# Kernel optimization log

Measured on AMD Instinct MI355X. Metric: run time of the kernel, lower is better.

## Reference

```python
import jax, jax.numpy as jnp
import numpy as np
from jax import lax

# SLAYER neuron / simulation constants (from netParams)
THETA = 10.0       # spike threshold
TAU_SR = 10.0      # synaptic (PSP) time constant
TAU_REF = 1.0      # refractory time constant
SCALE_REF = 2.0    # refractory scale
TAU_RHO = 1.0      # surrogate-gradient width (unused in fwd)
K_PSP = 32         # truncation length of SRM alpha kernel
K_REF = 16         # truncation length of refractory kernel

_t = np.arange(K_PSP, dtype=np.float64)
PSP_KERN = jnp.asarray((_t / TAU_SR) * np.exp(1.0 - _t / TAU_SR), jnp.float32)  # [K_PSP]
_tr = np.arange(1, K_REF + 1, dtype=np.float64)
REF_KERN = jnp.asarray(-SCALE_REF * THETA * (_tr / TAU_REF) * np.exp(1.0 - _tr / TAU_REF), jnp.float32)  # [K_REF]


def psp(x):
    """Causal temporal FIR filter with SRM alpha kernel; x: [..., T]."""
    sh = x.shape
    T = sh[-1]
    flat = x.reshape(-1, 1, T)                       # [B*, 1, T]
    k = PSP_KERN[::-1][None, None, :]                # correlation kernel (reversed)
    y = lax.conv_general_dilated(flat, k, (1,), [(K_PSP - 1, 0)])
    return y.reshape(sh)


def spike(u):
    """Threshold with refractory feedback, sequential over time. u: [..., T]."""
    uT = jnp.moveaxis(u, -1, 0)                      # [T, ...]
    buf0 = jnp.zeros(u.shape[:-1] + (K_REF,), u.dtype)

    def step(buf, ut):
        v = ut + buf[..., 0]
        s = (v >= THETA).astype(u.dtype)
        buf = jnp.concatenate([buf[..., 1:], jnp.zeros_like(buf[..., :1])], -1)
        buf = buf + s[..., None] * REF_KERN
        return buf, s

    _, sT = lax.scan(step, buf0, uT)
    return jnp.moveaxis(sT, 0, -1)


def conv_t(x, w, stride, pad):
    """2D conv applied independently per timestep. x: [N,C,H,W,T], w: [Co,C,kh,kw]."""
    N, C, H, W, T = x.shape
    xt = jnp.moveaxis(x, -1, 1).reshape(N * T, C, H, W)
    y = lax.conv_general_dilated(xt, w, (stride, stride), [(pad, pad), (pad, pad)])
    Co, Ho, Wo = y.shape[1], y.shape[2], y.shape[3]
    return jnp.moveaxis(y.reshape(N, T, Co, Ho, Wo), 1, -1)


def pool_t(x):
    """SLAYER sum-pool 2x2/s2 with weight 1.1*theta/kernel_area. x: [N,C,H,W,T]."""
    s = lax.reduce_window(x, np.float32(0.0), lax.add, (1, 1, 2, 2, 1), (1, 1, 2, 2, 1), 'VALID')
    return s * np.float32(1.1 * THETA / 4.0)


def setup_inputs() -> dict:
    key = jax.random.key(0)
    ks = jax.random.split(key, 5)
    spikeInput = (jax.random.uniform(ks[0], (4, 2, 256, 256, 50)) < 0.02).astype(jnp.float32)
    w1 = jax.random.normal(ks[1], (8, 2, 5, 5), jnp.float32) * 2.0
    w2 = jax.random.normal(ks[2], (16, 8, 3, 3), jnp.float32) * 1.5
    w3 = jax.random.normal(ks[3], (32, 16, 3, 3), jnp.float32) * 1.5
    w_fc = jax.random.normal(ks[4], (2, 32, 8, 8), jnp.float32) * 0.3
    return {"spikeInput": spikeInput, "w1": w1, "w2": w2, "w3": w3, "w_fc": w_fc}


def reference(spikeInput, w1, w2, w3, w_fc):
    x = spike(conv_t(psp(spikeInput), w1, 2, 1))   # [4,8,127,127,50]
    x = spike(pool_t(psp(x)))                      # [4,8,63,63,50]
    x = spike(conv_t(psp(x), w2, 2, 1))            # [4,16,32,32,50]
    x = spike(pool_t(psp(x)))                      # [4,16,16,16,50]
    x = spike(conv_t(psp(x), w3, 2, 1))            # [4,32,8,8,50]
    u = psp(x)
    out = jnp.einsum('ochw,nchwt->not', w_fc, u)   # dense over (C,H,W)
    return spike(out[:, :, None, None, :])         # [4,2,1,1,50]
```

## Files before the change

### kernel.cpp

```cpp
#include <hip/hip_runtime.h>
#include <cmath>

struct K32 { float k[32]; };
struct K16 { float k[16]; };

#define THETA 10.0f

__global__ __launch_bounds__(128)
void psp_kernel(const float* __restrict__ in, float* __restrict__ out,
                int nrows, K32 pk) {
  __shared__ __align__(16) float lds[64 * 50];
  const int rowBase = blockIdx.x * 64;
  const int tid = threadIdx.x;
  const int vr = min(64, nrows - rowBase);
  const int n4 = (vr * 50) >> 2;
  const float4* g4 = (const float4*)(in + (size_t)rowBase * 50);
  for (int i = tid; i < n4; i += 128) *(float4*)(&lds[4 * i]) = g4[i];
  __syncthreads();
  const int r = tid & 63;
  const int part = tid >> 6;
  const bool act = r < vr;
  float x[50];
  if (act) {
    if (part == 0) {
#pragma unroll
      for (int t = 0; t < 25; ++t) x[t] = lds[r * 50 + t];
    } else {
#pragma unroll
      for (int t = 0; t < 50; ++t) x[t] = lds[r * 50 + t];
    }
  }
  __syncthreads();
  if (act) {
    if (part == 0) {
#pragma unroll
      for (int t = 0; t < 25; ++t) {
        float a = 0.f;
#pragma unroll
        for (int k = 31; k >= 0; --k)
          if (t - k >= 0) a += x[t - k] * pk.k[k];
        lds[r * 50 + t] = a;
      }
    } else {
#pragma unroll
      for (int t = 25; t < 50; ++t) {
        float a = 0.f;
#pragma unroll
        for (int k = 31; k >= 0; --k)
          if (t - k >= 0) a += x[t - k] * pk.k[k];
        lds[r * 50 + t] = a;
      }
    }
  }
  __syncthreads();
  float4* o4 = (float4*)(out + (size_t)rowBase * 50);
  for (int i = tid; i < n4; i += 128) o4[i] = *(const float4*)(&lds[4 * i]);
}

template <int CIN, int COUT, int KK, int HIN, int WIN, int S1H, int S1W,
          int S2H, int S2W>
__global__ __launch_bounds__(256)
void conv_pps_kernel(const float* __restrict__ x, const float* __restrict__ w,
                     float* __restrict__ s2out, K32 pk, K16 rk) {
  constexpr int WT = 4;
  constexpr int SW = 8;
  constexpr int XR = 2 * (WT - 1) + KK;
  constexpr int GROUPS = (S1W + SW - 1) / SW;
  constexpr int NROW = COUT * 2 * SW;
  __shared__ float lds[NROW * 51];
  const int tid = threadIdx.x;
  const int wave = tid >> 6;
  const int lane = tid & 63;
  const int group = blockIdx.x % GROUPS;
  const int rest = blockIdx.x / GROUPS;
  const int hop = rest % S2H;
  const int n = rest / S2H;
  const int ho_off = wave & 1;
  const int wo_half = wave >> 1;
  const int ho = 2 * hop + ho_off;
  const int wo0 = group * SW + wo_half * WT;
  const int tt = lane < 50 ? lane : 49;

  float acc[COUT][WT] = {};
  for (int c = 0; c < CIN; ++c) {
#pragma unroll
    for (int kh = 0; kh < KK; ++kh) {
      const int hi = 2 * ho + kh - 1;
      if ((unsigned)hi >= (unsigned)HIN) continue;
      float xr[XR];
#pragma unroll
      for (int i = 0; i < XR; ++i) {
        const int wi = 2 * wo0 - 1 + i;
        xr[i] = ((unsigned)wi < (unsigned)WIN)
                    ? x[(((size_t)(n * CIN + c) * HIN + hi) * WIN + wi) * 50 + tt]
                    : 0.f;
      }
#pragma unroll
      for (int co = 0; co < COUT; ++co)
#pragma unroll
        for (int kw = 0; kw < KK; ++kw) {
          const float wv = w[((co * CIN + c) * KK + kh) * KK + kw];
#pragma unroll
          for (int wl = 0; wl < WT; ++wl)
            acc[co][wl] += xr[2 * wl + kw] * wv;
        }
    }
  }
  if (lane < 50) {
#pragma unroll
    for (int co = 0; co < COUT; ++co)
#pragma unroll
      for (int wl = 0; wl < WT; ++wl)
        lds[((co * 2 + ho_off) * SW + wo_half * WT + wl) * 51 + lane] = acc[co][wl];
  }
  __syncthreads();
  if (tid < NROW) {
    const int wol = tid & (SW - 1);
    if (group * SW + wol < S1W) {
      float buf[16];
#pragma unroll
      for (int j = 0; j < 16; ++j) buf[j] = 0.f;
#pragma unroll
      for (int t = 0; t < 50; ++t) {
        float v = lds[tid * 51 + t] + buf[t & 15];
        buf[t & 15] = 0.f;
        float sp = 0.f;
        if (v >= THETA) {
          sp = 1.f;
#pragma unroll
          for (int j = 0; j < 16; ++j) buf[(t + 1 + j) & 15] += rk.k[j];
        }
        lds[tid * 51 + t] = sp;
      }
    }
  }
  __syncthreads();
  {
    const int r = tid & (NROW - 1);
    const int part = tid >> 7;
    const int wol = r & (SW - 1);
    const bool act = (group * SW + wol) < S1W;
    float xs[50];
    if (act) {
      if (part == 0) {
#pragma unroll
        for (int t = 0; t < 25; ++t) xs[t] = lds[r * 51 + t];
      } else {
#pragma unroll
        for (int t = 0; t < 50; ++t) xs[t] = lds[r * 51 + t];
      }
    }
    __syncthreads();
    if (act) {
      if (part == 0) {
#pragma unroll
        for (int t = 0; t < 25; ++t) {
          float a = 0.f;
#pragma unroll
          for (int k = 31; k >= 0; --k)
            if (t - k >= 0) a += xs[t - k] * pk.k[k];
          lds[r * 51 + t] = a;
        }
      } else {
#pragma unroll
        for (int t = 25; t < 50; ++t) {
          float a = 0.f;
#pragma unroll
          for (int k = 31; k >= 0; --k)
            if (t - k >= 0) a += xs[t - k] * pk.k[k];
          lds[r * 51 + t] = a;
        }
      }
    }
  }
  __syncthreads();
  if (tid < COUT * (SW / 2)) {
    const int co = tid / (SW / 2);
    const int wpl = tid % (SW / 2);
    const int wop = group * (SW / 2) + wpl;
    if (wop < S2W) {
      const int r00 = (co * 16 + 2 * wpl) * 51;
      const int r01 = (co * 16 + 2 * wpl + 1) * 51;
      const int r10 = (co * 16 + 8 + 2 * wpl) * 51;
      const int r11 = (co * 16 + 8 + 2 * wpl + 1) * 51;
      float* orow = s2out + (((size_t)(n * COUT + co) * S2H + hop) * S2W + wop) * 50;
      float buf[16];
#pragma unroll
      for (int j = 0; j < 16; ++j) buf[j] = 0.f;
      float prev = 0.f;
#pragma unroll
      for (int t = 0; t < 50; ++t) {
        const float u0 = (((lds[r00 + t] + lds[r01 + t]) + lds[r10 + t]) + lds[r11 + t]) * 2.75f;
        float v = u0 + buf[t & 15];
        buf[t & 15] = 0.f;
        float sp = 0.f;
        if (v >= THETA) {
          sp = 1.f;
#pragma unroll
          for (int j = 0; j < 16; ++j) buf[(t + 1 + j) & 15] += rk.k[j];
        }
        if (t & 1) *(float2*)(orow + t - 1) = make_float2(prev, sp);
        else prev = sp;
      }
    }
  }
}

template <int CIN, int COUT, int KK, int WT, int HIN, int WIN, int HOUT, int WOUT>
__global__ __launch_bounds__(256)
void conv_spike_kernel(const float* __restrict__ x, const float* __restrict__ w,
                       float* __restrict__ s, K16 rk) {
  constexpr int XR = 2 * (WT - 1) + KK;
  constexpr int TW = 4 * WT;
  constexpr int GROUPS = (WOUT + TW - 1) / TW;
  __shared__ float lds[COUT * TW * 51];
  const int tid = threadIdx.x;
  const int wave = tid >> 6;
  const int lane = tid & 63;
  const int group = blockIdx.x % GROUPS;
  const int rest = blockIdx.x / GROUPS;
  const int ho = rest % HOUT;
  const int n = rest / HOUT;
  const int wo0 = group * TW + wave * WT;
  const int tt = lane < 50 ? lane : 49;

  float acc[COUT][WT] = {};
  for (int c = 0; c < CIN; ++c) {
#pragma unroll
    for (int kh = 0; kh < KK; ++kh) {
      const int hi = 2 * ho + kh - 1;
      if ((unsigned)hi >= (unsigned)HIN) continue;
      float xr[XR];
#pragma unroll
      for (int i = 0; i < XR; ++i) {
        const int wi = 2 * wo0 - 1 + i;
        xr[i] = ((unsigned)wi < (unsigned)WIN)
                    ? x[(((size_t)(n * CIN + c) * HIN + hi) * WIN + wi) * 50 + tt]
                    : 0.f;
      }
#pragma unroll
      for (int co = 0; co < COUT; ++co)
#pragma unroll
        for (int kw = 0; kw < KK; ++kw) {
          const float wv = w[((co * CIN + c) * KK + kh) * KK + kw];
#pragma unroll
          for (int wl = 0; wl < WT; ++wl)
            acc[co][wl] += xr[2 * wl + kw] * wv;
        }
    }
  }

  if (lane < 50) {
#pragma unroll
    for (int co = 0; co < COUT; ++co)
#pragma unroll
      for (int wl = 0; wl < WT; ++wl)
        lds[(co * TW + wave * WT + wl) * 51 + lane] = acc[co][wl];
  }
  __syncthreads();
  if (tid < COUT * TW) {
    const int co = tid / TW;
    const int wol = tid - co * TW;
    const int wo = group * TW + wol;
    if (wo < WOUT) {
      float* orow = s + (((size_t)(n * COUT + co) * HOUT + ho) * WOUT + wo) * 50;
      float buf[16];
#pragma unroll
      for (int j = 0; j < 16; ++j) buf[j] = 0.f;
      float prev = 0.f;
#pragma unroll
      for (int t = 0; t < 50; ++t) {
        float v = lds[tid * 51 + t] + buf[t & 15];
        buf[t & 15] = 0.f;
        float sp = 0.f;
        if (v >= THETA) {
          sp = 1.f;
#pragma unroll
          for (int j = 0; j < 16; ++j) buf[(t + 1 + j) & 15] += rk.k[j];
        }
        if (t & 1) *(float2*)(orow + t - 1) = make_float2(prev, sp);
        else prev = sp;
      }
    }
  }
}

__global__ __launch_bounds__(128)
void pps_kernel(const float* __restrict__ in, float* __restrict__ out,
                int Hin, int Win, int Hout, int Wout, int nseg,
                K32 pk, K16 rk) {
  __shared__ __align__(16) float lds[80 * 50];
  const int tid = threadIdx.x;
  const int seg = blockIdx.x % nseg;
  const int rest = blockIdx.x / nseg;
  const int ho = rest % Hout;
  const int nc = rest / Hout;
  const int wbase = seg * 32;
  const int nw = min(32, 2 * Wout - wbase);
  const int nwo = nw >> 1;
  const int span = nw * 50;
  const float* b0 = in + ((size_t)(nc * Hin + 2 * ho) * Win + wbase) * 50;
  const float* b1 = b0 + (size_t)Win * 50;
  const int n2 = span >> 1;
  for (int i = tid; i < n2; i += 128) {
    *(float2*)(&lds[2 * i]) = *(const float2*)(b0 + 2 * i);
    *(float2*)(&lds[span + 2 * i]) = *(const float2*)(b1 + 2 * i);
  }
  __syncthreads();
  const int r = tid & 63;
  const int part = tid >> 6;
  const bool act = r < 2 * nw;
  float x[50];
  if (act) {
    if (part == 0) {
#pragma unroll
      for (int t = 0; t < 25; ++t) x[t] = lds[r * 50 + t];
    } else {
#pragma unroll
      for (int t = 0; t < 50; ++t) x[t] = lds[r * 50 + t];
    }
  }
  __syncthreads();
  if (act) {
    if (part == 0) {
#pragma unroll
      for (int t = 0; t < 25; ++t) {
        float a = 0.f;
#pragma unroll
        for (int k = 31; k >= 0; --k)
          if (t - k >= 0) a += x[t - k] * pk.k[k];
        lds[r * 50 + t] = a;
      }
    } else {
#pragma unroll
      for (int t = 25; t < 50; ++t) {
        float a = 0.f;
#pragma unroll
        for (int k = 31; k >= 0; --k)
          if (t - k >= 0) a += x[t - k] * pk.k[k];
        lds[r * 50 + t] = a;
      }
    }
  }
  __syncthreads();
  if (tid < nwo) {
    float buf[16];
#pragma unroll
    for (int j = 0; j < 16; ++j) buf[j] = 0.f;
    const int r00 = (2 * tid) * 50, r01 = (2 * tid + 1) * 50;
    const int r10 = (nw + 2 * tid) * 50, r11 = (nw + 2 * tid + 1) * 50;
    const int ro = (2 * nw + tid) * 50;
#pragma unroll
    for (int t = 0; t < 50; ++t) {
      const float u0 = (((lds[r00 + t] + lds[r01 + t]) + lds[r10 + t]) + lds[r11 + t]) * 2.75f;
      float v = u0 + buf[t & 15];
      buf[t & 15] = 0.f;
      float sp = 0.f;
      if (v >= THETA) {
        sp = 1.f;
#pragma unroll
        for (int j = 0; j < 16; ++j) buf[(t + 1 + j) & 15] += rk.k[j];
      }
      lds[ro + t] = sp;
    }
  }
  __syncthreads();
  float* ob = out + ((size_t)(nc * Hout + ho) * Wout + seg * 16) * 50;
  const int base = 2 * nw * 50;
  for (int i = tid; i < nwo * 25; i += 128)
    *(float2*)(ob + 2 * i) = *(const float2*)(&lds[base + 2 * i]);
}

__global__ __launch_bounds__(512)
void fc_spike_kernel(const float* __restrict__ w, const float* __restrict__ u,
                     float* __restrict__ out, K16 rk) {
  __shared__ float lds[8 * 51];
  const int tid = threadIdx.x;
  const int wave = tid >> 6, lane = tid & 63;
  const int o = wave & 1, n = wave >> 1;
  const int tt = lane < 50 ? lane : 49;
  const float* wrow = w + (size_t)o * 2048;
  const float* ub = u + (size_t)n * 2048 * 50;
  float acc = 0.f;
#pragma unroll 32
  for (int i = 0; i < 2048; ++i) acc += wrow[i] * ub[(size_t)i * 50 + tt];
  if (lane < 50) lds[wave * 51 + lane] = acc;
  __syncthreads();
  if (tid < 8) {
    float buf[16];
#pragma unroll
    for (int j = 0; j < 16; ++j) buf[j] = 0.f;
#pragma unroll
    for (int t = 0; t < 50; ++t) {
      float v = lds[tid * 51 + t] + buf[t & 15];
      buf[t & 15] = 0.f;
      float sp = 0.f;
      if (v >= THETA) {
        sp = 1.f;
#pragma unroll
        for (int j = 0; j < 16; ++j) buf[(t + 1 + j) & 15] += rk.k[j];
      }
      out[tid * 50 + t] = sp;
    }
  }
}

extern "C" void kernel_launch(void* const* d_in, const int* in_sizes, int n_in,
                              void* d_out, int out_size, void* d_ws, size_t ws_size,
                              hipStream_t stream) {
  const float* xin = (const float*)d_in[0];
  const float* w1  = (const float*)d_in[1];
  const float* w2  = (const float*)d_in[2];
  const float* w3  = (const float*)d_in[3];
  const float* wfc = (const float*)d_in[4];
  float* out = (float*)d_out;

  float* R0 = (float*)d_ws;
  float* R1 = R0 + 26214400;

  K32 pk;
  for (int k = 0; k < 32; ++k)
    pk.k[k] = (float)(((double)k / 10.0) * exp(1.0 - (double)k / 10.0));
  K16 rk;
  for (int j = 0; j < 16; ++j) {
    const double tr = (double)(j + 1);
    rk.k[j] = (float)(-2.0 * 10.0 * tr * exp(1.0 - tr));
  }

  psp_kernel<<<8192, 128, 0, stream>>>(xin, R0, 524288, pk);
  conv_pps_kernel<2, 8, 5, 256, 256, 127, 127, 63, 63>
      <<<4 * 63 * 16, 256, 0, stream>>>(R0, w1, R1, pk, rk);
  psp_kernel<<<1985, 128, 0, stream>>>(R1, R0, 127008, pk);
  conv_spike_kernel<8, 16, 3, 1, 63, 63, 32, 32>
      <<<4 * 32 * 8, 256, 0, stream>>>(R0, w2, R1, rk);
  pps_kernel<<<4 * 16 * 16, 128, 0, stream>>>(R1, R0, 32, 32, 16, 16, 1, pk, rk);
  psp_kernel<<<256, 128, 0, stream>>>(R0, R1, 16384, pk);
  conv_spike_kernel<16, 32, 3, 1, 16, 16, 8, 8>
      <<<4 * 8 * 2, 256, 0, stream>>>(R1, w3, R0, rk);
  psp_kernel<<<128, 128, 0, stream>>>(R0, R1, 8192, pk);
  fc_spike_kernel<<<1, 512, 0, stream>>>(wfc, R1, out, rk);
}
```

Measured before the change: 506.4 us.

## Fuse input PSP filter into first conv kernel with LDS-staged input tile

Removes the standalone psp_kernel over the raw input and instead loads each block's input patch (CIN x 7 rows x 19 columns x 50 timesteps) into shared memory, applies the PSP FIR filter in place, then runs the conv from LDS rather than from global memory. This drops one full read and write of the large input tensor and replaces strided global gathers in the conv with LDS reads. In exchange, overlapping halo rows and columns are filtered redundantly across neighbouring blocks, and the kernel uses more LDS, which may lower occupancy.

```diff
diff --git a/kernel.cpp b/kernel.cpp
--- a/kernel.cpp
+++ b/kernel.cpp
@@ -67,7 +67,11 @@
   constexpr int XR = 2 * (WT - 1) + KK;
   constexpr int GROUPS = (S1W + SW - 1) / SW;
   constexpr int NROW = COUT * 2 * SW;
-  __shared__ float lds[NROW * 51];
+  constexpr int PH = KK + 2;
+  constexpr int PW = 2 * (SW - 1) + KK;
+  constexpr int PR = CIN * PH * PW;
+  constexpr int LDSF = (PR * 50 > NROW * 51) ? PR * 50 : NROW * 51;
+  __shared__ __align__(16) float lds[LDSF];
   const int tid = threadIdx.x;
   const int wave = tid >> 6;
   const int lane = tid & 63;
@@ -77,24 +81,75 @@
   const int n = rest / S2H;
   const int ho_off = wave & 1;
   const int wo_half = wave >> 1;
-  const int ho = 2 * hop + ho_off;
-  const int wo0 = group * SW + wo_half * WT;
   const int tt = lane < 50 ? lane : 49;
-
+  const int wi0 = 2 * group * SW - 1;
+
+  const float* xb = x + (size_t)n * CIN * HIN * WIN * 50;
+#pragma unroll
+  for (int sp = 0; sp < CIN * PH; ++sp) {
+    const int c = sp / PH, ph = sp - c * PH;
+    const int hi = 4 * hop - 1 + ph;
+    const bool hok = (unsigned)hi < (unsigned)HIN;
+    const float2* gp2 = (const float2*)(xb + (((long)c * HIN + hi) * (long)WIN + wi0) * 50);
+    const int lo = (wi0 < 0) ? 25 : 0;
+    const int hiE = (wi0 + PW > WIN) ? (WIN - wi0) * 25 : PW * 25;
+    float* dst = &lds[sp * PW * 50];
+    for (int e2 = tid; e2 < PW * 25; e2 += 256) {
+      float2 v = make_float2(0.f, 0.f);
+      if (hok && e2 >= lo && e2 < hiE) v = gp2[e2];
+      *(float2*)(dst + 2 * e2) = v;
+    }
+  }
+  __syncthreads();
+#pragma unroll
+  for (int base = 0; base < 2 * PR; base += 256) {
+    const int slot = base + tid;
+    const int r = slot >> 1;
+    const int part = slot & 1;
+    const bool act = r < PR;
+    float xs[50];
+    if (act) {
+      if (part == 0) {
+#pragma unroll
+        for (int t = 0; t < 25; ++t) xs[t] = lds[r * 50 + t];
+      } else {
+#pragma unroll
+        for (int t = 0; t < 50; ++t) xs[t] = lds[r * 50 + t];
+      }
+    }
+    __syncthreads();
+    if (act) {
+      if (part == 0) {
+#pragma unroll
+        for (int t = 0; t < 25; ++t) {
+          float a = 0.f;
+#pragma unroll
+          for (int k = 31; k >= 0; --k)
+            if (t - k >= 0) a += xs[t - k] * pk.k[k];
+          lds[r * 50 + t] = a;
+        }
+      } else {
+#pragma unroll
+        for (int t = 25; t < 50; ++t) {
+          float a = 0.f;
+#pragma unroll
+          for (int k = 31; k >= 0; --k)
+            if (t - k >= 0) a += xs[t - k] * pk.k[k];
+          lds[r * 50 + t] = a;
+        }
+      }
+    }
+    __syncthreads();
+  }
   float acc[COUT][WT] = {};
+#pragma unroll
   for (int c = 0; c < CIN; ++c) {
 #pragma unroll
     for (int kh = 0; kh < KK; ++kh) {
-      const int hi = 2 * ho + kh - 1;
-      if ((unsigned)hi >= (unsigned)HIN) continue;
+      const int rowb = (c * PH + 2 * ho_off + kh) * PW + 8 * wo_half;
       float xr[XR];
 #pragma unroll
-      for (int i = 0; i < XR; ++i) {
-        const int wi = 2 * wo0 - 1 + i;
-        xr[i] = ((unsigned)wi < (unsigned)WIN)
-                    ? x[(((size_t)(n * CIN + c) * HIN + hi) * WIN + wi) * 50 + tt]
-                    : 0.f;
-      }
+      for (int i = 0; i < XR; ++i) xr[i] = lds[(rowb + i) * 50 + tt];
 #pragma unroll
       for (int co = 0; co < COUT; ++co)
 #pragma unroll
@@ -106,6 +161,7 @@
         }
     }
   }
+  __syncthreads();
   if (lane < 50) {
 #pragma unroll
     for (int co = 0; co < COUT; ++co)
@@ -427,9 +483,8 @@
     rk.k[j] = (float)(-2.0 * 10.0 * tr * exp(1.0 - tr));
   }
 
-  psp_kernel<<<8192, 128, 0, stream>>>(xin, R0, 524288, pk);
   conv_pps_kernel<2, 8, 5, 256, 256, 127, 127, 63, 63>
-      <<<4 * 63 * 16, 256, 0, stream>>>(R0, w1, R1, pk, rk);
+      <<<4 * 63 * 16, 256, 0, stream>>>(xin, w1, R1, pk, rk);
   psp_kernel<<<1985, 128, 0, stream>>>(R1, R0, 127008, pk);
   conv_spike_kernel<8, 16, 3, 1, 63, 63, 32, 32>
       <<<4 * 32 * 8, 256, 0, stream>>>(R0, w2, R1, rk);
```

Result: slower. 562.9 us (+11.1%).

## Fuse trailing PSP filter into spike-producing kernels, dropping three psp launches

Applied to the files above, without the earlier changes.

The temporal PSP filter that followed each spike stage is now computed inside the producer kernels (conv_pps, pps, and the last conv_spike via a PSP_OUT template flag). Spikes are written to LDS, filtered in place by pairs of threads, and only the filtered potential is stored to global memory. This removes three standalone psp_kernel launches and their global read/write round trips. In exchange it adds extra LDS passes, barriers and register pressure (50-float arrays) to the fused kernels.

```diff
diff --git a/kernel.cpp b/kernel.cpp
--- a/kernel.cpp
+++ b/kernel.cpp
@@ -61,12 +61,13 @@
           int S2H, int S2W>
 __global__ __launch_bounds__(256)
 void conv_pps_kernel(const float* __restrict__ x, const float* __restrict__ w,
-                     float* __restrict__ s2out, K32 pk, K16 rk) {
+                     float* __restrict__ u3out, K32 pk, K16 rk) {
   constexpr int WT = 4;
   constexpr int SW = 8;
   constexpr int XR = 2 * (WT - 1) + KK;
   constexpr int GROUPS = (S1W + SW - 1) / SW;
   constexpr int NROW = COUT * 2 * SW;
+  constexpr int NOUT = COUT * (SW / 2);
   __shared__ float lds[NROW * 51];
   const int tid = threadIdx.x;
   const int wave = tid >> 6;
@@ -174,7 +175,7 @@
     }
   }
   __syncthreads();
-  if (tid < COUT * (SW / 2)) {
+  if (tid < NOUT) {
     const int co = tid / (SW / 2);
     const int wpl = tid % (SW / 2);
     const int wop = group * (SW / 2) + wpl;
@@ -183,11 +184,9 @@
       const int r01 = (co * 16 + 2 * wpl + 1) * 51;
       const int r10 = (co * 16 + 8 + 2 * wpl) * 51;
       const int r11 = (co * 16 + 8 + 2 * wpl + 1) * 51;
-      float* orow = s2out + (((size_t)(n * COUT + co) * S2H + hop) * S2W + wop) * 50;
       float buf[16];
 #pragma unroll
       for (int j = 0; j < 16; ++j) buf[j] = 0.f;
-      float prev = 0.f;
 #pragma unroll
       for (int t = 0; t < 50; ++t) {
         const float u0 = (((lds[r00 + t] + lds[r01 + t]) + lds[r10 + t]) + lds[r11 + t]) * 2.75f;
@@ -199,17 +198,73 @@
 #pragma unroll
           for (int j = 0; j < 16; ++j) buf[(t + 1 + j) & 15] += rk.k[j];
         }
-        if (t & 1) *(float2*)(orow + t - 1) = make_float2(prev, sp);
-        else prev = sp;
-      }
+        lds[r00 + t] = sp;
+      }
+    }
+  }
+  __syncthreads();
+  {
+    const int r = tid >> 1;
+    const int part = tid & 1;
+    const int co = r / (SW / 2);
+    const int wpl = r % (SW / 2);
+    const bool act = (r < NOUT) && (group * (SW / 2) + wpl < S2W);
+    const int row = (co * 16 + 2 * wpl) * 51;
+    float xs[50];
+    if (act) {
+      if (part == 0) {
+#pragma unroll
+        for (int t = 0; t < 25; ++t) xs[t] = lds[row + t];
+      } else {
+#pragma unroll
+        for (int t = 0; t < 50; ++t) xs[t] = lds[row + t];
+      }
+    }
+    __syncthreads();
+    if (act) {
+      if (part == 0) {
+#pragma unroll
+        for (int t = 0; t < 25; ++t) {
+          float a = 0.f;
+#pragma unroll
+          for (int k = 31; k >= 0; --k)
+            if (t - k >= 0) a += xs[t - k] * pk.k[k];
+          lds[row + t] = a;
+        }
+      } else {
+#pragma unroll
+        for (int t = 25; t < 50; ++t) {
+          float a = 0.f;
+#pragma unroll
+          for (int k = 31; k >= 0; --k)
+            if (t - k >= 0) a += xs[t - k] * pk.k[k];
+          lds[row + t] = a;
+        }
+      }
+    }
+  }
+  __syncthreads();
+  for (int i2 = tid; i2 < NOUT * 25; i2 += 256) {
+    const int r = i2 / 25;
+    const int j = i2 - r * 25;
+    const int co = r / (SW / 2);
+    const int wpl = r % (SW / 2);
+    const int wop = group * (SW / 2) + wpl;
+    if (wop < S2W) {
+      const int row = (co * 16 + 2 * wpl) * 51;
+      float2 v;
+      v.x = lds[row + 2 * j];
+      v.y = lds[row + 2 * j + 1];
+      *(float2*)(u3out + (((size_t)(n * COUT + co) * S2H + hop) * S2W + wop) * 50 + 2 * j) = v;
     }
   }
 }
 
-template <int CIN, int COUT, int KK, int WT, int HIN, int WIN, int HOUT, int WOUT>
+template <int CIN, int COUT, int KK, int WT, int HIN, int WIN, int HOUT, int WOUT,
+          bool PSP_OUT>
 __global__ __launch_bounds__(256)
 void conv_spike_kernel(const float* __restrict__ x, const float* __restrict__ w,
-                       float* __restrict__ s, K16 rk) {
+                       float* __restrict__ s, K32 pk, K16 rk) {
   constexpr int XR = 2 * (WT - 1) + KK;
   constexpr int TW = 4 * WT;
   constexpr int GROUPS = (WOUT + TW - 1) / TW;
@@ -258,28 +313,106 @@
         lds[(co * TW + wave * WT + wl) * 51 + lane] = acc[co][wl];
   }
   __syncthreads();
-  if (tid < COUT * TW) {
-    const int co = tid / TW;
-    const int wol = tid - co * TW;
-    const int wo = group * TW + wol;
-    if (wo < WOUT) {
-      float* orow = s + (((size_t)(n * COUT + co) * HOUT + ho) * WOUT + wo) * 50;
-      float buf[16];
-#pragma unroll
-      for (int j = 0; j < 16; ++j) buf[j] = 0.f;
-      float prev = 0.f;
-#pragma unroll
-      for (int t = 0; t < 50; ++t) {
-        float v = lds[tid * 51 + t] + buf[t & 15];
-        buf[t & 15] = 0.f;
-        float sp = 0.f;
-        if (v >= THETA) {
-          sp = 1.f;
-#pragma unroll
-          for (int j = 0; j < 16; ++j) buf[(t + 1 + j) & 15] += rk.k[j];
-        }
-        if (t & 1) *(float2*)(orow + t - 1) = make_float2(prev, sp);
-        else prev = sp;
+
+  if constexpr (!PSP_OUT) {
+    if (tid < COUT * TW) {
+      const int co = tid / TW;
+      const int wol = tid - co * TW;
+      const int wo = group * TW + wol;
+      if (wo < WOUT) {
+        float* orow = s + (((size_t)(n * COUT + co) * HOUT + ho) * WOUT + wo) * 50;
+        float buf[16];
+#pragma unroll
+        for (int j = 0; j < 16; ++j) buf[j] = 0.f;
+        float prev = 0.f;
+#pragma unroll
+        for (int t = 0; t < 50; ++t) {
+          float v = lds[tid * 51 + t] + buf[t & 15];
+          buf[t & 15] = 0.f;
+          float sp = 0.f;
+          if (v >= THETA) {
+            sp = 1.f;
+#pragma unroll
+            for (int j = 0; j < 16; ++j) buf[(t + 1 + j) & 15] += rk.k[j];
+          }
+          if (t & 1) *(float2*)(orow + t - 1) = make_float2(prev, sp);
+          else prev = sp;
+        }
+      }
+    }
+  } else {
+    if (tid < COUT * TW) {
+      const int wol = tid % TW;
+      if (group * TW + wol < WOUT) {
+        float buf[16];
+#pragma unroll
+        for (int j = 0; j < 16; ++j) buf[j] = 0.f;
+#pragma unroll
+        for (int t = 0; t < 50; ++t) {
+          float v = lds[tid * 51 + t] + buf[t & 15];
+          buf[t & 15] = 0.f;
+          float sp = 0.f;
+          if (v >= THETA) {
+            sp = 1.f;
+#pragma unroll
+            for (int j = 0; j < 16; ++j) buf[(t + 1 + j) & 15] += rk.k[j];
+          }
+          lds[tid * 51 + t] = sp;
+        }
+      }
+    }
+    __syncthreads();
+    {
+      const int r = tid % (COUT * TW);
+      const int part = tid / (COUT * TW);
+      const int wol = r % TW;
+      const bool act = (tid < 2 * COUT * TW) && (group * TW + wol < WOUT);
+      float xs[50];
+      if (act) {
+        if (part == 0) {
+#pragma unroll
+          for (int t = 0; t < 25; ++t) xs[t] = lds[r * 51 + t];
+        } else {
+#pragma unroll
+          for (int t = 0; t < 50; ++t) xs[t] = lds[r * 51 + t];
+        }
+      }
+      __syncthreads();
+      if (act) {
+        if (part == 0) {
+#pragma unroll
+          for (int t = 0; t < 25; ++t) {
+            float a = 0.f;
+#pragma unroll
+            for (int k = 31; k >= 0; --k)
+              if (t - k >= 0) a += xs[t - k] * pk.k[k];
+            lds[r * 51 + t] = a;
+          }
+        } else {
+#pragma unroll
+          for (int t = 25; t < 50; ++t) {
+            float a = 0.f;
+#pragma unroll
+            for (int k = 31; k >= 0; --k)
+              if (t - k >= 0) a += xs[t - k] * pk.k[k];
+            lds[r * 51 + t] = a;
+          }
+        }
+      }
+    }
+    __syncthreads();
+    constexpr int PER2 = TW * 25;
+    for (int i2 = tid; i2 < COUT * PER2; i2 += 256) {
+      const int co = i2 / PER2;
+      const int r2 = i2 - co * PER2;
+      const int wol = r2 / 25;
+      const int j = r2 - wol * 25;
+      const int wo = group * TW + wol;
+      if (wo < WOUT) {
+        float2 v;
+        v.x = lds[(co * TW + wol) * 51 + 2 * j];
+        v.y = lds[(co * TW + wol) * 51 + 2 * j + 1];
+        *(float2*)(s + (((size_t)(n * COUT + co) * HOUT + ho) * WOUT + wo) * 50 + 2 * j) = v;
       }
     }
   }
@@ -307,38 +440,40 @@
     *(float2*)(&lds[span + 2 * i]) = *(const float2*)(b1 + 2 * i);
   }
   __syncthreads();
-  const int r = tid & 63;
-  const int part = tid >> 6;
-  const bool act = r < 2 * nw;
-  float x[50];
-  if (act) {
-    if (part == 0) {
-#pragma unroll
-      for (int t = 0; t < 25; ++t) x[t] = lds[r * 50 + t];
-    } else {
-#pragma unroll
-      for (int t = 0; t < 50; ++t) x[t] = lds[r * 50 + t];
-    }
-  }
-  __syncthreads();
-  if (act) {
-    if (part == 0) {
-#pragma unroll
-      for (int t = 0; t < 25; ++t) {
-        float a = 0.f;
-#pragma unroll
-        for (int k = 31; k >= 0; --k)
-          if (t - k >= 0) a += x[t - k] * pk.k[k];
-        lds[r * 50 + t] = a;
-      }
-    } else {
-#pragma unroll
-      for (int t = 25; t < 50; ++t) {
-        float a = 0.f;
-#pragma unroll
-        for (int k = 31; k >= 0; --k)
-          if (t - k >= 0) a += x[t - k] * pk.k[k];
-        lds[r * 50 + t] = a;
+  {
+    const int r = tid & 63;
+    const int part = tid >> 6;
+    const bool act = r < 2 * nw;
+    float x[50];
+    if (act) {
+      if (part == 0) {
+#pragma unroll
+        for (int t = 0; t < 25; ++t) x[t] = lds[r * 50 + t];
+      } else {
+#pragma unroll
+        for (int t = 0; t < 50; ++t) x[t] = lds[r * 50 + t];
+      }
+    }
+    __syncthreads();
+    if (act) {
+      if (part == 0) {
+#pragma unroll
+        for (int t = 0; t < 25; ++t) {
+          float a = 0.f;
+#pragma unroll
+          for (int k = 31; k >= 0; --k)
+            if (t - k >= 0) a += x[t - k] * pk.k[k];
+          lds[r * 50 + t] = a;
+        }
+      } else {
+#pragma unroll
+        for (int t = 25; t < 50; ++t) {
+          float a = 0.f;
+#pragma unroll
+          for (int k = 31; k >= 0; --k)
+            if (t - k >= 0) a += x[t - k] * pk.k[k];
+          lds[r * 50 + t] = a;
+        }
       }
     }
   }
@@ -362,6 +497,45 @@
         for (int j = 0; j < 16; ++j) buf[(t + 1 + j) & 15] += rk.k[j];
       }
       lds[ro + t] = sp;
+    }
+  }
+  __syncthreads();
+  {
+    const int r = tid >> 1;
+    const int part = tid & 1;
+    const bool act = r < nwo;
+    const int row = (2 * nw + r) * 50;
+    float xs[50];
+    if (act) {
+      if (part == 0) {
+#pragma unroll
+        for (int t = 0; t < 25; ++t) xs[t] = lds[row + t];
+      } else {
+#pragma unroll
+        for (int t = 0; t < 50; ++t) xs[t] = lds[row + t];
+      }
+    }
+    __syncthreads();
+    if (act) {
+      if (part == 0) {
+#pragma unroll
+        for (int t = 0; t < 25; ++t) {
+          float a = 0.f;
+#pragma unroll
+          for (int k = 31; k >= 0; --k)
+            if (t - k >= 0) a += xs[t - k] * pk.k[k];
+          lds[row + t] = a;
+        }
+      } else {
+#pragma unroll
+        for (int t = 25; t < 50; ++t) {
+          float a = 0.f;
+#pragma unroll
+          for (int k = 31; k >= 0; --k)
+            if (t - k >= 0) a += xs[t - k] * pk.k[k];
+          lds[row + t] = a;
+        }
+      }
     }
   }
   __syncthreads();
@@ -430,13 +604,10 @@
   psp_kernel<<<8192, 128, 0, stream>>>(xin, R0, 524288, pk);
   conv_pps_kernel<2, 8, 5, 256, 256, 127, 127, 63, 63>
       <<<4 * 63 * 16, 256, 0, stream>>>(R0, w1, R1, pk, rk);
-  psp_kernel<<<1985, 128, 0, stream>>>(R1, R0, 127008, pk);
-  conv_spike_kernel<8, 16, 3, 1, 63, 63, 32, 32>
-      <<<4 * 32 * 8, 256, 0, stream>>>(R0, w2, R1, rk);
-  pps_kernel<<<4 * 16 * 16, 128, 0, stream>>>(R1, R0, 32, 32, 16, 16, 1, pk, rk);
-  psp_kernel<<<256, 128, 0, stream>>>(R0, R1, 16384, pk);
-  conv_spike_kernel<16, 32, 3, 1, 16, 16, 8, 8>
-      <<<4 * 8 * 2, 256, 0, stream>>>(R1, w3, R0, rk);
-  psp_kernel<<<128, 128, 0, stream>>>(R0, R1, 8192, pk);
-  fc_spike_kernel<<<1, 512, 0, stream>>>(wfc, R1, out, rk);
+  conv_spike_kernel<8, 16, 3, 1, 63, 63, 32, 32, false>
+      <<<4 * 32 * 8, 256, 0, stream>>>(R1, w2, R0, pk, rk);
+  pps_kernel<<<4 * 16 * 16, 128, 0, stream>>>(R0, R1, 32, 32, 16, 16, 1, pk, rk);
+  conv_spike_kernel<16, 32, 3, 1, 16, 16, 8, 8, true>
+      <<<4 * 8 * 2, 256, 0, stream>>>(R1, w3, R0, pk, rk);
+  fc_spike_kernel<<<1, 512, 0, stream>>>(wfc, R0, out, rk);
 }
```

After: 507.4 us. About the same (+0.2%).
